# Optimization experiments

Hardware: AMD Instinct MI355X
Metric: run time of the kernel (lower is better)

## Reference

```python
import jax, jax.numpy as jnp
import numpy as np

B, S, D, H, F = 4, 1024, 512, 8, 2048
EPS = 1e-6


def _layernorm(x, g, b):
    m = jnp.mean(x, axis=-1, keepdims=True)
    v = jnp.mean(jnp.square(x - m), axis=-1, keepdims=True)
    return (x - m) * jax.lax.rsqrt(v + EPS) * g + b


def setup_inputs() -> dict:
    key = jax.random.key(0)
    ks = jax.random.split(key, 16)
    sd = 0.02
    return {
        "input_tensor": jax.random.normal(ks[0], (B, S, D), jnp.float32),
        # per-head QKV projections: each head maps D -> D (full depth, as in source)
        "Wq": jax.random.normal(ks[1], (H, D, D), jnp.float32) * sd,
        "bq": jnp.zeros((H, D), jnp.float32),
        "Wk": jax.random.normal(ks[2], (H, D, D), jnp.float32) * sd,
        "bk": jnp.zeros((H, D), jnp.float32),
        "Wv": jax.random.normal(ks[3], (H, D, D), jnp.float32) * sd,
        "bv": jnp.zeros((H, D), jnp.float32),
        # output projection after concat of H full-depth heads: (H*D) -> D
        "Wo": jax.random.normal(ks[4], (H * D, D), jnp.float32) * sd,
        "bo": jnp.zeros((D,), jnp.float32),
        "g1": jnp.ones((D,), jnp.float32),
        "beta1": jnp.zeros((D,), jnp.float32),
        "W1": jax.random.normal(ks[5], (D, F), jnp.float32) * sd,
        "b1": jnp.zeros((F,), jnp.float32),
        "W2": jax.random.normal(ks[6], (F, D), jnp.float32) * sd,
        "b2": jnp.zeros((D,), jnp.float32),
        "g2": jnp.ones((D,), jnp.float32),
        "beta2": jnp.zeros((D,), jnp.float32),
    }


def reference(input_tensor, Wq, bq, Wk, bk, Wv, bv, Wo, bo,
              g1, beta1, W1, b1, W2, b2, g2, beta2):
    x = input_tensor
    # batched per-head projections: [B,S,D] x [H,D,E] -> [B,H,S,E]
    q = jnp.einsum("bsd,hde->bhse", x, Wq) + bq[None, :, None, :]
    k = jnp.einsum("bsd,hde->bhse", x, Wk) + bk[None, :, None, :]
    v = jnp.einsum("bsd,hde->bhse", x, Wv) + bv[None, :, None, :]
    scale = 1.0 / jnp.sqrt(jnp.asarray(D, x.dtype))
    scores = jnp.einsum("bhse,bhte->bhst", q, k) * scale  # [B,H,S,S]
    attn = jax.nn.softmax(scores, axis=-1)
    heads = jnp.einsum("bhst,bhte->bhse", attn, v)  # [B,H,S,E]
    # concat heads on last axis: [B,S,H*D]
    concat = jnp.transpose(heads, (0, 2, 1, 3)).reshape(B, S, H * D)
    mha = concat @ Wo + bo  # [B,S,D]
    # dropout is identity at inference
    y = _layernorm(x + mha, g1, beta1)
    ff = jax.nn.relu(y @ W1 + b1) @ W2 + b2
    return _layernorm(y + ff, g2, beta2)
```

## Files before the change

kernel.cpp:

```cpp
#include <hip/hip_runtime.h>
#include <hip/hip_bf16.h>

typedef unsigned short u16;
typedef unsigned int u32;
typedef __attribute__((ext_vector_type(4))) float f32x4;
typedef __attribute__((ext_vector_type(8))) __bf16 bf16x8;

#define DEV __device__ __forceinline__

DEV u16 f2bf(float f) {
  union { float f; unsigned u; } c; c.f = f;
  unsigned r = (c.u + 0x7fffu + ((c.u >> 16) & 1u)) >> 16;
  return (u16)r;
}

DEV void gld_lds16(const void* g, void* l) {
  __builtin_amdgcn_global_load_lds(
      (__attribute__((address_space(1))) void*)g,
      (__attribute__((address_space(3))) void*)l, 16, 0, 0);
}

DEV f32x4 mfma_bf16(bf16x8 a, bf16x8 b, f32x4 c) {
  return __builtin_amdgcn_mfma_f32_16x16x32_bf16(a, b, c, 0, 0, 0);
}

DEV void bar_vm0() { asm volatile("s_waitcnt vmcnt(0) lgkmcnt(0)\n\ts_barrier" ::: "memory"); }
DEV void wait_lg0() { asm volatile("s_waitcnt lgkmcnt(0)" ::: "memory"); }

DEV u32 cvt_pk_bf16(float lo, float hi) {
  u32 d;
  asm("v_cvt_pk_bf16_f32 %0, %1, %2" : "=v"(d) : "v"(lo), "v"(hi));
  return d;
}

__global__ __launch_bounds__(256) void prep_kernel(const float* __restrict__ x,
                                                   const float* __restrict__ Wq,
                                                   const float* __restrict__ Wk,
                                                   const float* __restrict__ Wv,
                                                   const float* __restrict__ Wo,
                                                   const float* __restrict__ W1,
                                                   const float* __restrict__ W2,
                                                   u16* __restrict__ xb, u16* __restrict__ wqT,
                                                   u16* __restrict__ wkT, u16* __restrict__ wvT,
                                                   u16* __restrict__ woT, u16* __restrict__ w1T,
                                                   u16* __restrict__ w2T) {
  int b = blockIdx.x;
  int tid = threadIdx.x;
  if (b < 2048) {
    int i = b * 256 + tid;
    float4 v = ((const float4*)x)[i];
    ushort4 o;
    o.x = f2bf(v.x); o.y = f2bf(v.y); o.z = f2bf(v.z); o.w = f2bf(v.w);
    ((ushort4*)xb)[i] = o;
    return;
  }
  int idx = b - 2048;
  const float* in;
  u16* out;
  int R, C, bx, by, bz = 0;
  if (idx < 6144) {
    int job = idx >> 11;
    in = job == 0 ? Wq : (job == 1 ? Wk : Wv);
    out = job == 0 ? wqT : (job == 1 ? wkT : wvT);
    int rr = idx & 2047;
    bz = rr >> 8;
    by = (rr >> 4) & 15;
    bx = rr & 15;
    R = 512; C = 512;
  } else if (idx < 8192) {
    int rr = idx - 6144;
    in = Wo; out = woT; R = 4096; C = 512;
    by = rr >> 4; bx = rr & 15;
  } else if (idx < 9216) {
    int rr = idx - 8192;
    in = W1; out = w1T; R = 512; C = 2048;
    by = rr >> 6; bx = rr & 63;
  } else {
    int rr = idx - 9216;
    in = W2; out = w2T; R = 2048; C = 512;
    by = rr >> 4; bx = rr & 15;
  }
  __shared__ float t[32][33];
  size_t base = (size_t)bz * R * C;
  const float* ip = in + base;
  u16* op = out + base;
  int c0 = bx * 32, r0 = by * 32;
  int tx = tid & 31, ty = tid >> 5;
#pragma unroll
  for (int i = 0; i < 4; ++i) {
    int rr2 = ty + i * 8;
    t[rr2][tx] = ip[(size_t)(r0 + rr2) * C + c0 + tx];
  }
  __syncthreads();
#pragma unroll
  for (int i = 0; i < 4; ++i) {
    int cc = ty + i * 8;
    op[(size_t)(c0 + cc) * R + r0 + tx] = f2bf(t[tx][cc]);
  }
}

template <int NT, int BM, int BN, int WM, int WN, int MODE>
__global__ __launch_bounds__(NT) void gemm_tn(const u16* __restrict__ A,
                                              const u16* __restrict__ B, int N, int K,
                                              void* __restrict__ out0, void* __restrict__ out1,
                                              const float* __restrict__ bias0,
                                              const float* __restrict__ bias1) {
  constexpr int BK = 64;
  constexpr int MF = WM / 16, NF = WN / 16;
  constexpr int WC = BN / WN;
  constexpr int AI = (BM * BK / 8) / NT;
  constexpr int BI = (BN * BK / 8) / NT;
  __shared__ u16 As[2][BM * BK];
  __shared__ u16 Bs[2][BN * BK];
  const int tid = threadIdx.x;
  const int wave = tid >> 6, lane = tid & 63;
  const int r = lane & 15, g = lane >> 4;
  const int row0 = blockIdx.y * BM, col0 = blockIdx.x * BN;
  const int wr = (wave / WC) * WM, wc = (wave % WC) * WN;

  auto stage = [&](int kt, int p) {
#pragma unroll
    for (int i = 0; i < AI; ++i) {
      int bi = i * NT + wave * 64;
      int c = bi + lane;
      int row = c >> 3, ch = (c & 7) ^ (row & 7);
      gld_lds16(A + (size_t)(row0 + row) * K + kt + ch * 8, &As[p][(size_t)bi * 8]);
    }
#pragma unroll
    for (int i = 0; i < BI; ++i) {
      int bi = i * NT + wave * 64;
      int c = bi + lane;
      int row = c >> 3, ch = (c & 7) ^ (row & 7);
      gld_lds16(B + (size_t)(col0 + row) * K + kt + ch * 8, &Bs[p][(size_t)bi * 8]);
    }
  };

  f32x4 acc[MF][NF] = {};
  const int nt = K / BK;

  stage(0, 0);
  for (int t = 0; t < nt; ++t) {
    const int p = t & 1;
    bar_vm0();
    if (t + 1 < nt) stage((t + 1) * BK, p ^ 1);
    __builtin_amdgcn_s_setprio(1);
#pragma unroll
    for (int kk = 0; kk < 2; ++kk) {
      bf16x8 af[MF], bfv[NF];
#pragma unroll
      for (int m = 0; m < MF; ++m)
        af[m] = *(const bf16x8*)(&As[p][(wr + m * 16 + r) * BK + (((kk * 4 + g) ^ (r & 7))) * 8]);
#pragma unroll
      for (int n = 0; n < NF; ++n)
        bfv[n] = *(const bf16x8*)(&Bs[p][(wc + n * 16 + r) * BK + (((kk * 4 + g) ^ (r & 7))) * 8]);
#pragma unroll
      for (int m = 0; m < MF; ++m)
#pragma unroll
        for (int n = 0; n < NF; ++n)
          acc[m][n] = mfma_bf16(af[m], bfv[n], acc[m][n]);
    }
    __builtin_amdgcn_s_setprio(0);
  }

#pragma unroll
  for (int m = 0; m < MF; ++m) {
#pragma unroll
    for (int n = 0; n < NF; ++n) {
      int gcol = col0 + wc + n * 16 + r;
#pragma unroll
      for (int j = 0; j < 4; ++j) {
        int grow = row0 + wr + m * 16 + g * 4 + j;
        float val = acc[m][n][j];
        if constexpr (MODE == 0) {
          int ph = gcol >> 12;
          int he = gcol & 4095;
          u16* dst = (u16*)(ph ? out1 : out0);
          const float* bsp = ph ? bias1 : bias0;
          val += bsp[he];
          int bb = grow >> 10, s = grow & 1023;
          size_t off = (((size_t)(bb * 8 + (he >> 9)) * 1024 + s) * 512) + (he & 511);
          dst[off] = f2bf(val);
        } else if constexpr (MODE == 1) {
          val += bias0[grow];
          int bb = gcol >> 10, s = gcol & 1023;
          size_t off = (((size_t)bb * 8 + (grow >> 9)) * 512 + (grow & 511)) * 1024 + s;
          ((u16*)out0)[off] = f2bf(val);
        } else if constexpr (MODE == 2) {
          ((float*)out0)[(size_t)grow * N + gcol] = val + bias0[gcol];
        } else {
          float v2 = fmaxf(val + bias0[gcol], 0.0f);
          ((u16*)out0)[(size_t)grow * N + gcol] = f2bf(v2);
        }
      }
    }
  }
  (void)out1; (void)bias1;
}

__global__ __launch_bounds__(512, 2) void flash_kernel(const u16* __restrict__ qg,
                                                       const u16* __restrict__ kg,
                                                       const u16* __restrict__ vtg,
                                                       u16* __restrict__ concat) {
  constexpr float SCALE = 0.04419417382415922f;
  __shared__ u16 Ks[2][32 * 512];
  __shared__ u16 Vs[2][32 * 512];
  __shared__ u32 PsU[8][256];

  const int tid = threadIdx.x;
  const int wave = tid >> 6, lane = tid & 63;
  const int r = lane & 15, g = lane >> 4;
  const int bx = blockIdx.x;
  const int xcd = bx & 7, slot = bx >> 3;
  const int bh = xcd * 4 + (slot >> 3);
  const int qt = slot & 7;
  const int bb = bh >> 3, hh = bh & 7;
  const size_t hbase = (size_t)bh * 1024 * 512;
  const u16* qp = qg + hbase;
  const u16* kp = kg + hbase;
  const u16* vp = vtg + hbase;
  const int q0 = qt * 128;

  bf16x8 q[16];
#pragma unroll
  for (int kk = 0; kk < 16; ++kk)
    q[kk] = *(const bf16x8*)(qp + (size_t)(q0 + wave * 16 + r) * 512 + kk * 32 + g * 8);

  const int krow8 = lane >> 3, kch = (lane & 7) ^ (lane >> 3);
  const int vrow4 = lane >> 2, vch = (lane & 3) ^ ((lane >> 3) & 3);
  auto stageKV = [&](int t, int p) {
    int kv = t * 32;
#pragma unroll
    for (int j = 0; j < 4; ++j) {
      int id = wave * 4 + j;
      gld_lds16(kp + (size_t)(kv + j * 8 + krow8) * 512 + wave * 64 + kch * 8,
                &Ks[p][id * 512]);
    }
#pragma unroll
    for (int j = 0; j < 4; ++j) {
      int n = wave * 4 + j;
      gld_lds16(vp + (size_t)(n * 16 + vrow4) * 1024 + kv + vch * 8, &Vs[p][n * 512]);
    }
  };

  f32x4 o[32] = {};
  float mrun = -1e30f, lrun = 0.f;

  stageKV(0, 0);

  const int krh = (r >> 3) * 512;
  const int ke0 = (r & 7) * 64 + ((g ^ (r & 7)) * 8);
  const int ke1 = (r & 7) * 64 + (((4 + g) ^ (r & 7)) * 8);
  const int voff = (r * 4 + (g ^ ((r >> 1) & 3))) * 8;

  for (int t = 0; t < 32; ++t) {
    const int p = t & 1;
    bar_vm0();
    if (t < 31) stageKV(t + 1, p ^ 1);

    __builtin_amdgcn_s_setprio(1);
    f32x4 a0 = {}, a1 = {}, b0 = {}, b1 = {};
#pragma unroll
    for (int kc = 0; kc < 8; ++kc) {
      const u16* kb = &Ks[p][kc * 2048 + krh];
      bf16x8 kf00 = *(const bf16x8*)(kb + ke0);
      bf16x8 kf01 = *(const bf16x8*)(kb + 1024 + ke0);
      bf16x8 kf10 = *(const bf16x8*)(kb + ke1);
      bf16x8 kf11 = *(const bf16x8*)(kb + 1024 + ke1);
      a0 = mfma_bf16(kf00, q[2 * kc], a0);
      b0 = mfma_bf16(kf01, q[2 * kc], b0);
      a1 = mfma_bf16(kf10, q[2 * kc + 1], a1);
      b1 = mfma_bf16(kf11, q[2 * kc + 1], b1);
    }
    __builtin_amdgcn_s_setprio(0);
    f32x4 s0 = a0 + a1;
    f32x4 s1 = b0 + b1;

    float m8 = -1e30f;
#pragma unroll
    for (int j = 0; j < 4; ++j) {
      s0[j] *= SCALE;
      s1[j] *= SCALE;
      m8 = fmaxf(m8, fmaxf(s0[j], s1[j]));
    }
    m8 = fmaxf(m8, __shfl_xor(m8, 16));
    m8 = fmaxf(m8, __shfl_xor(m8, 32));
    if (__any(m8 - mrun > 6.0f)) {
      float mn = fmaxf(mrun, m8);
      float rs = __expf(mrun - mn);
      mrun = mn;
      lrun *= rs;
#pragma unroll
      for (int j = 0; j < 4; ++j) {
        float rsj = __shfl(rs, (lane & 48) | (g * 4 + j));
#pragma unroll
        for (int n = 0; n < 32; ++n) o[n][j] *= rsj;
      }
    }
    f32x4 p0, p1;
    float ls = 0.f;
#pragma unroll
    for (int j = 0; j < 4; ++j) {
      p0[j] = __expf(s0[j] - mrun);
      p1[j] = __expf(s1[j] - mrun);
      ls += p0[j] + p1[j];
    }
    ls += __shfl_xor(ls, 16);
    ls += __shfl_xor(ls, 32);
    lrun += ls;

    {
      u32* pw = &PsU[wave][0];
      int base = r * 4 + (g & 1) * 2 + (g >> 1) * 64;
      pw[base + 0] = cvt_pk_bf16(p0[0], p0[1]);
      pw[base + 1] = cvt_pk_bf16(p0[2], p0[3]);
      pw[base + 128 + 0] = cvt_pk_bf16(p1[0], p1[1]);
      pw[base + 128 + 1] = cvt_pk_bf16(p1[2], p1[3]);
    }
    wait_lg0();

    bf16x8 pa = *(const bf16x8*)&PsU[wave][lane * 4];
    __builtin_amdgcn_s_setprio(1);
#pragma unroll
    for (int n = 0; n < 32; ++n) {
      bf16x8 bv = *(const bf16x8*)&Vs[p][n * 512 + voff];
      o[n] = mfma_bf16(pa, bv, o[n]);
    }
    __builtin_amdgcn_s_setprio(0);
  }

  float invl = 1.0f / lrun;
#pragma unroll
  for (int j = 0; j < 4; ++j) {
    float inv = __shfl(invl, (lane & 48) | (g * 4 + j));
    int srow = q0 + wave * 16 + g * 4 + j;
    size_t rowoff = ((size_t)bb * 1024 + srow) * 4096;
#pragma unroll
    for (int n = 0; n < 32; ++n) {
      int ocol = hh * 512 + n * 16 + r;
      concat[rowoff + ocol] = f2bf(o[n][j] * inv);
    }
  }
}

__global__ __launch_bounds__(128) void add_ln_kernel(const float* __restrict__ xin,
                                                     const float* __restrict__ addin,
                                                     const float* __restrict__ gamma,
                                                     const float* __restrict__ beta,
                                                     float* __restrict__ yout,
                                                     u16* __restrict__ ybout) {
  int row = blockIdx.x;
  int t = threadIdx.x;
  float4 xv = ((const float4*)(xin + (size_t)row * 512))[t];
  float4 av = ((const float4*)(addin + (size_t)row * 512))[t];
  float v0 = xv.x + av.x, v1 = xv.y + av.y, v2 = xv.z + av.z, v3 = xv.w + av.w;
  float s1 = v0 + v1 + v2 + v3;
  float s2 = v0 * v0 + v1 * v1 + v2 * v2 + v3 * v3;
#pragma unroll
  for (int d = 1; d < 64; d <<= 1) {
    s1 += __shfl_xor(s1, d);
    s2 += __shfl_xor(s2, d);
  }
  __shared__ float sh[4];
  int wv = t >> 6;
  if ((t & 63) == 0) { sh[wv * 2] = s1; sh[wv * 2 + 1] = s2; }
  __syncthreads();
  s1 = sh[0] + sh[2];
  s2 = sh[1] + sh[3];
  float mean = s1 * (1.0f / 512.0f);
  float var = s2 * (1.0f / 512.0f) - mean * mean;
  float rstd = rsqrtf(var + 1e-6f);
  float4 gv = ((const float4*)gamma)[t];
  float4 bv = ((const float4*)beta)[t];
  float o0 = (v0 - mean) * rstd * gv.x + bv.x;
  float o1 = (v1 - mean) * rstd * gv.y + bv.y;
  float o2 = (v2 - mean) * rstd * gv.z + bv.z;
  float o3 = (v3 - mean) * rstd * gv.w + bv.w;
  float4 ov; ov.x = o0; ov.y = o1; ov.z = o2; ov.w = o3;
  ((float4*)(yout + (size_t)row * 512))[t] = ov;
  if (ybout) {
    ushort4 ub;
    ub.x = f2bf(o0); ub.y = f2bf(o1); ub.z = f2bf(o2); ub.w = f2bf(o3);
    ((ushort4*)(ybout + (size_t)row * 512))[t] = ub;
  }
}

extern "C" void kernel_launch(void* const* d_in, const int* in_sizes, int n_in, void* d_out,
                              int out_size, void* d_ws, size_t ws_size, hipStream_t stream) {
  (void)in_sizes; (void)n_in; (void)out_size; (void)ws_size;
  const float* x   = (const float*)d_in[0];
  const float* Wq  = (const float*)d_in[1];
  const float* bq  = (const float*)d_in[2];
  const float* Wk  = (const float*)d_in[3];
  const float* bk  = (const float*)d_in[4];
  const float* Wv  = (const float*)d_in[5];
  const float* bv  = (const float*)d_in[6];
  const float* Wo  = (const float*)d_in[7];
  const float* bo  = (const float*)d_in[8];
  const float* g1  = (const float*)d_in[9];
  const float* be1 = (const float*)d_in[10];
  const float* W1  = (const float*)d_in[11];
  const float* b1  = (const float*)d_in[12];
  const float* W2  = (const float*)d_in[13];
  const float* b2  = (const float*)d_in[14];
  const float* g2  = (const float*)d_in[15];
  const float* be2 = (const float*)d_in[16];

  char* ws = (char*)d_ws;
  const size_t MB = 1024 * 1024;
  u16*   xb   = (u16*)(ws + 0);
  u16*   wqkT = (u16*)(ws + 4 * MB);
  u16*   wvT  = (u16*)(ws + 12 * MB);
  u16*   woT  = (u16*)(ws + 16 * MB);
  u16*   w1T  = (u16*)(ws + 20 * MB);
  u16*   w2T  = (u16*)(ws + 22 * MB);
  u16*   qb   = (u16*)(ws + 24 * MB);
  u16*   kb   = (u16*)(ws + 56 * MB);
  u16*   vTb  = (u16*)(ws + 88 * MB);
  u16*   cc   = (u16*)(ws + 120 * MB);
  float* mha  = (float*)(ws + 24 * MB);
  float* y    = (float*)(ws + 32 * MB);
  u16*   yb   = (u16*)(ws + 40 * MB);
  u16*   ff1  = (u16*)(ws + 56 * MB);
  float* ff2  = (float*)(ws + 72 * MB);

  prep_kernel<<<12288, 256, 0, stream>>>(x, Wq, Wk, Wv, Wo, W1, W2, xb, wqkT,
                                         wqkT + 8 * 512 * 512, wvT, woT, w1T, w2T);

  gemm_tn<512, 256, 256, 128, 64, 0><<<dim3(32, 16), 512, 0, stream>>>(xb, wqkT, 8192, 512, qb, kb, bq, bk);
  gemm_tn<512, 256, 256, 128, 64, 1><<<dim3(16, 16), 512, 0, stream>>>(wvT, xb, 4096, 512, vTb, nullptr, bv, nullptr);
  flash_kernel<<<256, 512, 0, stream>>>(qb, kb, vTb, cc);
  gemm_tn<256, 64, 128, 32, 64, 2><<<dim3(4, 64), 256, 0, stream>>>(cc, woT, 512, 4096, mha, nullptr, bo, nullptr);
  add_ln_kernel<<<4096, 128, 0, stream>>>(x, mha, g1, be1, y, yb);
  gemm_tn<256, 128, 128, 64, 64, 3><<<dim3(16, 32), 256, 0, stream>>>(yb, w1T, 2048, 512, ff1, nullptr, b1, nullptr);
  gemm_tn<256, 64, 128, 32, 64, 2><<<dim3(4, 64), 256, 0, stream>>>(ff1, w2T, 512, 2048, ff2, nullptr, b2, nullptr);
  add_ln_kernel<<<4096, 128, 0, stream>>>(y, ff2, g2, be2, (float*)d_out, nullptr);
}
```

Measured before the change: 293.9 us.

## Split-K output and FFN2 GEMMs and share V tiles across wave pairs in flash

The Wo and W2 GEMMs now split K in two across blockIdx.z. Each half writes a separate fp32 partial buffer, and the following add+layernorm kernel sums both partials, which doubles the block count for these 256-block launches. In the flash kernel, each wave pair now processes two query tiles against half of the V columns, so each V fragment read from LDS feeds two MFMAs. Rescale factors and running sums are exchanged through shared memory, which adds a block barrier per KV step. The split-K path adds extra fp32 partial traffic, and the barrier adds synchronisation cost.

```diff
diff --git a/kernel.cpp b/kernel.cpp
--- a/kernel.cpp
+++ b/kernel.cpp
@@ -25,7 +25,7 @@
 }
 
 DEV void bar_vm0() { asm volatile("s_waitcnt vmcnt(0) lgkmcnt(0)\n\ts_barrier" ::: "memory"); }
-DEV void wait_lg0() { asm volatile("s_waitcnt lgkmcnt(0)" ::: "memory"); }
+DEV void bar_lg0() { asm volatile("s_waitcnt lgkmcnt(0)\n\ts_barrier" ::: "memory"); }
 
 DEV u32 cvt_pk_bf16(float lo, float hi) {
   u32 d;
@@ -99,7 +99,7 @@
   }
 }
 
-template <int NT, int BM, int BN, int WM, int WN, int MODE>
+template <int NT, int BM, int BN, int WM, int WN, int MODE, int SPLITK>
 __global__ __launch_bounds__(NT) void gemm_tn(const u16* __restrict__ A,
                                               const u16* __restrict__ B, int N, int K,
                                               void* __restrict__ out0, void* __restrict__ out1,
@@ -117,6 +117,8 @@
   const int r = lane & 15, g = lane >> 4;
   const int row0 = blockIdx.y * BM, col0 = blockIdx.x * BN;
   const int wr = (wave / WC) * WM, wc = (wave % WC) * WN;
+  const int KS = K * SPLITK;
+  const int kb0 = blockIdx.z * K;
 
   auto stage = [&](int kt, int p) {
 #pragma unroll
@@ -124,14 +126,14 @@
       int bi = i * NT + wave * 64;
       int c = bi + lane;
       int row = c >> 3, ch = (c & 7) ^ (row & 7);
-      gld_lds16(A + (size_t)(row0 + row) * K + kt + ch * 8, &As[p][(size_t)bi * 8]);
+      gld_lds16(A + (size_t)(row0 + row) * KS + kb0 + kt + ch * 8, &As[p][(size_t)bi * 8]);
     }
 #pragma unroll
     for (int i = 0; i < BI; ++i) {
       int bi = i * NT + wave * 64;
       int c = bi + lane;
       int row = c >> 3, ch = (c & 7) ^ (row & 7);
-      gld_lds16(B + (size_t)(col0 + row) * K + kt + ch * 8, &Bs[p][(size_t)bi * 8]);
+      gld_lds16(B + (size_t)(col0 + row) * KS + kb0 + kt + ch * 8, &Bs[p][(size_t)bi * 8]);
     }
   };
 
@@ -162,6 +164,7 @@
     __builtin_amdgcn_s_setprio(0);
   }
 
+  const size_t moff = (size_t)blockIdx.z * gridDim.y * BM * N;
 #pragma unroll
   for (int m = 0; m < MF; ++m) {
 #pragma unroll
@@ -186,7 +189,8 @@
           size_t off = (((size_t)bb * 8 + (grow >> 9)) * 512 + (grow & 511)) * 1024 + s;
           ((u16*)out0)[off] = f2bf(val);
         } else if constexpr (MODE == 2) {
-          ((float*)out0)[(size_t)grow * N + gcol] = val + bias0[gcol];
+          if (SPLITK == 1 || blockIdx.z == 0) val += bias0[gcol];
+          ((float*)out0)[moff + (size_t)grow * N + gcol] = val;
         } else {
           float v2 = fmaxf(val + bias0[gcol], 0.0f);
           ((u16*)out0)[(size_t)grow * N + gcol] = f2bf(v2);
@@ -205,10 +209,13 @@
   __shared__ u16 Ks[2][32 * 512];
   __shared__ u16 Vs[2][32 * 512];
   __shared__ u32 PsU[8][256];
+  __shared__ float rsBuf[8][16];
+  __shared__ float wgmBuf[8];
 
   const int tid = threadIdx.x;
   const int wave = tid >> 6, lane = tid & 63;
   const int r = lane & 15, g = lane >> 4;
+  const int u = wave >> 1, s = wave & 1;
   const int bx = blockIdx.x;
   const int xcd = bx & 7, slot = bx >> 3;
   const int bh = xcd * 4 + (slot >> 3);
@@ -242,7 +249,7 @@
     }
   };
 
-  f32x4 o[32] = {};
+  f32x4 o[2][16] = {};
   float mrun = -1e30f, lrun = 0.f;
 
   stageKV(0, 0);
@@ -284,18 +291,20 @@
     }
     m8 = fmaxf(m8, __shfl_xor(m8, 16));
     m8 = fmaxf(m8, __shfl_xor(m8, 32));
-    if (__any(m8 - mrun > 6.0f)) {
+    float dm = m8 - mrun;
+    dm = fmaxf(dm, __shfl_xor(dm, 1));
+    dm = fmaxf(dm, __shfl_xor(dm, 2));
+    dm = fmaxf(dm, __shfl_xor(dm, 4));
+    dm = fmaxf(dm, __shfl_xor(dm, 8));
+    if (dm > 6.0f) {
       float mn = fmaxf(mrun, m8);
       float rs = __expf(mrun - mn);
+      if (g == 0) rsBuf[wave][r] = rs;
       mrun = mn;
       lrun *= rs;
-#pragma unroll
-      for (int j = 0; j < 4; ++j) {
-        float rsj = __shfl(rs, (lane & 48) | (g * 4 + j));
-#pragma unroll
-        for (int n = 0; n < 32; ++n) o[n][j] *= rsj;
-      }
-    }
+    }
+    if (lane == 0) wgmBuf[wave] = dm;
+
     f32x4 p0, p1;
     float ls = 0.f;
 #pragma unroll
@@ -316,34 +325,58 @@
       pw[base + 128 + 0] = cvt_pk_bf16(p1[0], p1[1]);
       pw[base + 128 + 1] = cvt_pk_bf16(p1[2], p1[3]);
     }
-    wait_lg0();
-
-    bf16x8 pa = *(const bf16x8*)&PsU[wave][lane * 4];
+    bar_lg0();
+
+    if (wgmBuf[2 * u] > 6.0f) {
+#pragma unroll
+      for (int j = 0; j < 4; ++j) {
+        float rj = rsBuf[2 * u][g * 4 + j];
+#pragma unroll
+        for (int n = 0; n < 16; ++n) o[0][n][j] *= rj;
+      }
+    }
+    if (wgmBuf[2 * u + 1] > 6.0f) {
+#pragma unroll
+      for (int j = 0; j < 4; ++j) {
+        float rj = rsBuf[2 * u + 1][g * 4 + j];
+#pragma unroll
+        for (int n = 0; n < 16; ++n) o[1][n][j] *= rj;
+      }
+    }
+
+    bf16x8 pa0 = *(const bf16x8*)&PsU[2 * u][lane * 4];
+    bf16x8 pa1 = *(const bf16x8*)&PsU[2 * u + 1][lane * 4];
     __builtin_amdgcn_s_setprio(1);
 #pragma unroll
-    for (int n = 0; n < 32; ++n) {
-      bf16x8 bv = *(const bf16x8*)&Vs[p][n * 512 + voff];
-      o[n] = mfma_bf16(pa, bv, o[n]);
+    for (int n = 0; n < 16; ++n) {
+      bf16x8 bv = *(const bf16x8*)&Vs[p][(s * 16 + n) * 512 + voff];
+      o[0][n] = mfma_bf16(pa0, bv, o[0][n]);
+      o[1][n] = mfma_bf16(pa1, bv, o[1][n]);
     }
     __builtin_amdgcn_s_setprio(0);
   }
 
-  float invl = 1.0f / lrun;
-#pragma unroll
-  for (int j = 0; j < 4; ++j) {
-    float inv = __shfl(invl, (lane & 48) | (g * 4 + j));
-    int srow = q0 + wave * 16 + g * 4 + j;
-    size_t rowoff = ((size_t)bb * 1024 + srow) * 4096;
-#pragma unroll
-    for (int n = 0; n < 32; ++n) {
-      int ocol = hh * 512 + n * 16 + r;
-      concat[rowoff + ocol] = f2bf(o[n][j] * inv);
+  if (g == 0) rsBuf[wave][r] = lrun;
+  __syncthreads();
+#pragma unroll
+  for (int qs = 0; qs < 2; ++qs) {
+#pragma unroll
+    for (int j = 0; j < 4; ++j) {
+      float inv = 1.0f / rsBuf[2 * u + qs][g * 4 + j];
+      int srow = q0 + u * 32 + qs * 16 + g * 4 + j;
+      size_t rowoff = ((size_t)bb * 1024 + srow) * 4096;
+#pragma unroll
+      for (int n = 0; n < 16; ++n) {
+        int ocol = hh * 512 + s * 256 + n * 16 + r;
+        concat[rowoff + ocol] = f2bf(o[qs][n][j] * inv);
+      }
     }
   }
 }
 
 __global__ __launch_bounds__(128) void add_ln_kernel(const float* __restrict__ xin,
                                                      const float* __restrict__ addin,
+                                                     const float* __restrict__ addin2,
                                                      const float* __restrict__ gamma,
                                                      const float* __restrict__ beta,
                                                      float* __restrict__ yout,
@@ -353,6 +386,10 @@
   float4 xv = ((const float4*)(xin + (size_t)row * 512))[t];
   float4 av = ((const float4*)(addin + (size_t)row * 512))[t];
   float v0 = xv.x + av.x, v1 = xv.y + av.y, v2 = xv.z + av.z, v3 = xv.w + av.w;
+  if (addin2) {
+    float4 bv2 = ((const float4*)(addin2 + (size_t)row * 512))[t];
+    v0 += bv2.x; v1 += bv2.y; v2 += bv2.z; v3 += bv2.w;
+  }
   float s1 = v0 + v1 + v2 + v3;
   float s2 = v0 * v0 + v1 * v1 + v2 * v2 + v3 * v3;
 #pragma unroll
@@ -417,21 +454,23 @@
   u16*   kb   = (u16*)(ws + 56 * MB);
   u16*   vTb  = (u16*)(ws + 88 * MB);
   u16*   cc   = (u16*)(ws + 120 * MB);
-  float* mha  = (float*)(ws + 24 * MB);
-  float* y    = (float*)(ws + 32 * MB);
-  u16*   yb   = (u16*)(ws + 40 * MB);
+  float* mha0 = (float*)(ws + 24 * MB);
+  float* mha1 = (float*)(ws + 32 * MB);
+  float* y    = (float*)(ws + 40 * MB);
+  u16*   yb   = (u16*)(ws + 48 * MB);
   u16*   ff1  = (u16*)(ws + 56 * MB);
-  float* ff2  = (float*)(ws + 72 * MB);
+  float* ff2a = (float*)(ws + 72 * MB);
+  float* ff2b = (float*)(ws + 80 * MB);
 
   prep_kernel<<<12288, 256, 0, stream>>>(x, Wq, Wk, Wv, Wo, W1, W2, xb, wqkT,
                                          wqkT + 8 * 512 * 512, wvT, woT, w1T, w2T);
 
-  gemm_tn<512, 256, 256, 128, 64, 0><<<dim3(32, 16), 512, 0, stream>>>(xb, wqkT, 8192, 512, qb, kb, bq, bk);
-  gemm_tn<512, 256, 256, 128, 64, 1><<<dim3(16, 16), 512, 0, stream>>>(wvT, xb, 4096, 512, vTb, nullptr, bv, nullptr);
+  gemm_tn<512, 256, 256, 128, 64, 0, 1><<<dim3(32, 16), 512, 0, stream>>>(xb, wqkT, 8192, 512, qb, kb, bq, bk);
+  gemm_tn<512, 256, 256, 128, 64, 1, 1><<<dim3(16, 16), 512, 0, stream>>>(wvT, xb, 4096, 512, vTb, nullptr, bv, nullptr);
   flash_kernel<<<256, 512, 0, stream>>>(qb, kb, vTb, cc);
-  gemm_tn<256, 64, 128, 32, 64, 2><<<dim3(4, 64), 256, 0, stream>>>(cc, woT, 512, 4096, mha, nullptr, bo, nullptr);
-  add_ln_kernel<<<4096, 128, 0, stream>>>(x, mha, g1, be1, y, yb);
-  gemm_tn<256, 128, 128, 64, 64, 3><<<dim3(16, 32), 256, 0, stream>>>(yb, w1T, 2048, 512, ff1, nullptr, b1, nullptr);
-  gemm_tn<256, 64, 128, 32, 64, 2><<<dim3(4, 64), 256, 0, stream>>>(ff1, w2T, 512, 2048, ff2, nullptr, b2, nullptr);
-  add_ln_kernel<<<4096, 128, 0, stream>>>(y, ff2, g2, be2, (float*)d_out, nullptr);
-}
+  gemm_tn<256, 64, 128, 32, 64, 2, 2><<<dim3(4, 64, 2), 256, 0, stream>>>(cc, woT, 512, 2048, mha0, nullptr, bo, nullptr);
+  add_ln_kernel<<<4096, 128, 0, stream>>>(x, mha0, mha1, g1, be1, y, yb);
+  gemm_tn<256, 128, 128, 64, 64, 3, 1><<<dim3(16, 32), 256, 0, stream>>>(yb, w1T, 2048, 512, ff1, nullptr, b1, nullptr);
+  gemm_tn<256, 64, 128, 32, 64, 2, 2><<<dim3(4, 64, 2), 256, 0, stream>>>(ff1, w2T, 512, 1024, ff2a, nullptr, b2, nullptr);
+  add_ln_kernel<<<4096, 128, 0, stream>>>(y, ff2a, ff2b, g2, be2, (float*)d_out, nullptr);
+}
```

Result: faster. 280.0 us (-4.7%).
